# Kernel optimization log

Measured on AMD Instinct MI355X. Metric: run time of the kernel, lower is better.

Reference implementation:

```python
import jax, jax.numpy as jnp
import numpy as np

HEADS = 16
ROPE_BASE = 10000.0


def _rope(x):
    # x: [B, S, D]; rotate interleaved even/odd pairs across full D
    B, S, D = x.shape
    half = D // 2
    inv_freq = 1.0 / (ROPE_BASE ** (jnp.arange(half, dtype=jnp.float32) * 2.0 / D))
    ang = jnp.arange(S, dtype=jnp.float32)[:, None] * inv_freq[None, :]  # [S, half]
    cos, sin = jnp.cos(ang), jnp.sin(ang)
    xp = x.reshape(B, S, half, 2)
    xe, xo = xp[..., 0], xp[..., 1]
    re = xe * cos - xo * sin
    ro = xe * sin + xo * cos
    return jnp.stack([re, ro], axis=-1).reshape(B, S, D)


def setup_inputs() -> dict:
    key = jax.random.key(0)
    ks = jax.random.split(key, 7)
    B, S, D = 2, 2048, 1024
    sc = 1.0 / np.sqrt(D)
    return {
        "queries": jax.random.normal(ks[0], (B, S, D), jnp.float32),
        "keys": jax.random.normal(ks[1], (B, S, D), jnp.float32),
        "values": jax.random.normal(ks[2], (B, S, D), jnp.float32),
        "Wq": jax.random.normal(ks[3], (D, D), jnp.float32) * sc,
        "Wk": jax.random.normal(ks[4], (D, D), jnp.float32) * sc,
        "Wv": jax.random.normal(ks[5], (D, D), jnp.float32) * sc,
        "Wo": jax.random.normal(ks[6], (D, D), jnp.float32) * sc,
    }


def reference(queries, keys, values, Wq, Wk, Wv, Wo):
    B, S, D = queries.shape
    H = HEADS
    dk = D // H
    # bias-free linear projections (torch Linear: x @ W^T)
    q = _rope(queries @ Wq.T)
    k = _rope(keys @ Wk.T)
    v = _rope(values @ Wv.T)
    # split heads: [B, H, S, dk]
    q = q.reshape(B, S, H, dk).transpose(0, 2, 1, 3)
    k = k.reshape(B, S, H, dk).transpose(0, 2, 1, 3)
    v = v.reshape(B, S, H, dk).transpose(0, 2, 1, 3)
    scores = jnp.einsum("bhqd,bhkd->bhqk", q, k) / jnp.sqrt(jnp.float32(dk))
    attn = jax.nn.softmax(scores, axis=-1)
    ctx = jnp.einsum("bhqk,bhkd->bhqd", attn, v)  # [B, H, S, dk]
    z = ctx.transpose(0, 2, 1, 3).reshape(B, S, D)
    return z @ Wo.T
```

## Files before the change

kernel.cpp:

```cpp
#include <hip/hip_runtime.h>
#include <hip/hip_bf16.h>
#include <math.h>


typedef __attribute__((ext_vector_type(8))) short s8v;
typedef __attribute__((ext_vector_type(8))) __bf16 bf16x8;
typedef __attribute__((ext_vector_type(4))) float f32x4;
typedef __attribute__((ext_vector_type(16))) float f32x16;
typedef __attribute__((ext_vector_type(2))) unsigned u32x2;

__device__ inline unsigned short f2bf(float f) {
    unsigned u = __builtin_bit_cast(unsigned, f);
    u += 0x7FFFu + ((u >> 16) & 1u);
    return (unsigned short)(u >> 16);
}

__device__ inline unsigned pk_bf16(float a, float b) {
    __hip_bfloat162 h = __float22bfloat162_rn(float2{a, b});
    unsigned u;
    __builtin_memcpy(&u, &h, 4);
    return u;
}

__device__ inline f32x4 mfma16(s8v a, s8v b, f32x4 c) {
    return __builtin_amdgcn_mfma_f32_16x16x32_bf16(
        __builtin_bit_cast(bf16x8, a), __builtin_bit_cast(bf16x8, b), c, 0, 0, 0);
}

__device__ inline f32x16 mfma32(s8v a, s8v b, f32x16 c) {
    return __builtin_amdgcn_mfma_f32_32x32x16_bf16(
        __builtin_bit_cast(bf16x8, a), __builtin_bit_cast(bf16x8, b), c, 0, 0, 0);
}

struct CvtArgs {
    const float* s[7];
    unsigned short* d[7];
    int n4[7];
};

__global__ __launch_bounds__(256) void cvt_kernel(CvtArgs a) {
    const int which = blockIdx.y;
    const float4* __restrict__ src = (const float4*)a.s[which];
    unsigned short* __restrict__ dst = a.d[which];
    const int n4 = a.n4[which];
    for (int i = blockIdx.x * 256 + threadIdx.x; i < n4; i += gridDim.x * 256) {
        float4 v = src[i];
        uint2 o;
        o.x = pk_bf16(v.x, v.y);
        o.y = pk_bf16(v.z, v.w);
        *(uint2*)(dst + (size_t)i * 4) = o;
    }
}

__global__ __launch_bounds__(256) void rope_table_kernel(float* __restrict__ cosT,
                                                         float* __restrict__ sinT) {
    int i = blockIdx.x * 256 + threadIdx.x;
    int s = i >> 9, d2 = i & 511;
    float inv = exp2f((float)d2 * (-13.287712379549449f / 512.0f));
    float ang = (float)s * inv;
    float sn, cs;
    sincosf(ang, &sn, &cs);
    cosT[i] = cs;
    sinT[i] = sn;
}

struct GemmArgs {
    const unsigned short* A[3];
    const unsigned short* W[3];
    void* C[3];
    const float* cosT;
    const float* sinT;
    float scale[3];
};

template <bool ROPE>
__global__ __launch_bounds__(256) void gemm_bt(GemmArgs g) {
    constexpr int K = 1024, N = 1024;
    const int z = blockIdx.z;
    const unsigned short* __restrict__ A = g.A[z];
    const unsigned short* __restrict__ W = g.W[z];

    const int tid = threadIdx.x;
    const int lane = tid & 63, wid = tid >> 6;
    const int wr = wid >> 1, wc = wid & 1;
    const int row0 = blockIdx.x * 128, col0 = blockIdx.y * 128;
    const int lr = lane & 15, kofs = (lane >> 4) * 8;

    __shared__ __align__(16) unsigned short As[128][72];
    __shared__ __align__(16) unsigned short Ws[128][72];

    f32x4 acc[4][4] = {};

    const int srow = tid >> 3;
    const int schunk = (tid & 7) * 8;

    for (int k0 = 0; k0 < K; k0 += 64) {
        __syncthreads();
#pragma unroll
        for (int i = 0; i < 4; ++i) {
            int r = srow + i * 32;
            *(s8v*)(&As[r][schunk]) =
                *(const s8v*)(A + (size_t)(row0 + r) * K + k0 + schunk);
            *(s8v*)(&Ws[r][schunk]) =
                *(const s8v*)(W + (size_t)(col0 + r) * K + k0 + schunk);
        }
        __syncthreads();

        s8v af[2][4], bf[2][4];
#pragma unroll
        for (int ks = 0; ks < 2; ++ks) {
#pragma unroll
            for (int m = 0; m < 4; ++m)
                af[ks][m] = *(const s8v*)(&As[wr * 64 + m * 16 + lr][ks * 32 + kofs]);
#pragma unroll
            for (int n = 0; n < 4; ++n)
                bf[ks][n] = *(const s8v*)(&Ws[wc * 64 + n * 16 + lr][ks * 32 + kofs]);
        }
#pragma unroll
        for (int m = 0; m < 4; ++m)
#pragma unroll
            for (int n = 0; n < 4; ++n) {
                acc[m][n] = mfma16(af[0][m], bf[0][n], acc[m][n]);
                acc[m][n] = mfma16(af[1][m], bf[1][n], acc[m][n]);
            }
    }

    const int rbase = row0 + wr * 64 + ((lane >> 4) << 2);
    const int cbase = col0 + wc * 64 + lr;
    const float scale = g.scale[z];
#pragma unroll
    for (int m = 0; m < 4; ++m) {
#pragma unroll
        for (int n = 0; n < 4; ++n) {
            const int gc = cbase + n * 16;
#pragma unroll
            for (int r = 0; r < 4; ++r) {
                const int gr = rbase + m * 16 + r;
                float v = acc[m][n][r];
                if constexpr (ROPE) {
                    const int s = gr & 2047;
                    const int d2 = gc >> 1;
                    float cs = g.cosT[s * 512 + d2];
                    float sn = g.sinT[s * 512 + d2];
                    float partner = __shfl_xor(v, 1);
                    v = (v * cs + partner * ((lane & 1) ? sn : -sn)) * scale;
                    ((unsigned short*)g.C[z])[(size_t)gr * N + gc] = f2bf(v);
                } else {
                    ((float*)g.C[z])[(size_t)gr * N + gc] = v;
                }
            }
        }
    }
}

__global__ __launch_bounds__(512, 2) void attn_kernel(
    const unsigned short* __restrict__ Q,
    const unsigned short* __restrict__ Km,
    const unsigned short* __restrict__ Vm,
    unsigned short* __restrict__ ctx) {
    const int tid = threadIdx.x;
    const int lane = tid & 63;
    const int w = tid >> 6;
    const int hi = lane >> 5;
    const int lq = lane & 31;
    const int qt = blockIdx.x;
    const int bh = blockIdx.y;
    const size_t base = (size_t)(bh >> 4) * 2048 * 1024;
    const int hcol = (bh & 15) * 64;
    const int q0 = qt * 256 + w * 32;

    __shared__ __align__(16) unsigned short Vt[2][64][72];

    const int vkey = tid >> 3;
    const int vc = tid & 7;
    const int vphys = ((((vkey >> 3) ^ vc) << 3) | (vkey & 7));

    auto stageV = [&](int buf, s8v vv) {
#pragma unroll
        for (int j = 0; j < 8; ++j)
            Vt[buf][vc * 8 + j][vphys] = (unsigned short)vv[j];
    };

    const unsigned short* __restrict__ Kp = Km + base + (size_t)lq * 1024 + hcol + hi * 8;
    const unsigned short* __restrict__ Vp = Vm + base + (size_t)vkey * 1024 + hcol + vc * 8;

    s8v qf[4];
#pragma unroll
    for (int s = 0; s < 4; ++s)
        qf[s] = *(const s8v*)(Q + base + (size_t)(q0 + lq) * 1024 + hcol + s * 16 + hi * 8);

    s8v kfA[8], kfB[8];
#pragma unroll
    for (int i = 0; i < 8; ++i)
        kfA[i] = *(const s8v*)(Kp + (size_t)((i >> 2) * 32) * 1024 + (i & 3) * 16);

    stageV(0, *(const s8v*)Vp);
    __syncthreads();

    f32x16 accO0 = {}, accO1 = {};
    float lacc = 0.f;

#define ATTN_STEP(KT, CUR, KFC, KFN)                                            \
    {                                                                           \
        const int kt_ = (KT);                                                   \
        const bool pre_ = (kt_ + 64 < 2048);                                    \
        s8v vnxt_;                                                              \
        if (pre_) {                                                             \
            vnxt_ = *(const s8v*)(Vp + (size_t)(kt_ + 64) * 1024);              \
            _Pragma("unroll")                                                   \
            for (int i = 0; i < 8; ++i)                                         \
                KFN[i] = *(const s8v*)(Kp +                                     \
                    (size_t)(kt_ + 64 + (i >> 2) * 32) * 1024 + (i & 3) * 16);  \
        }                                                                       \
                                       \
        f32x16 s0 = {}, s1 = {};                                                \
        _Pragma("unroll")                                                       \
        for (int s = 0; s < 4; ++s) {                                           \
            s0 = mfma32(KFC[s], qf[s], s0);                                     \
            s1 = mfma32(KFC[4 + s], qf[s], s1);                                 \
        }                                                                       \
           \
        s8v vf[8];                                                              \
        _Pragma("unroll")                                                       \
        for (int db = 0; db < 2; ++db)                                          \
            _Pragma("unroll")                                                   \
            for (int ks = 0; ks < 4; ++ks)                                      \
                vf[db * 4 + ks] = *(const s8v*)&Vt[CUR][db * 32 + lq]           \
                    [((2 * ks + hi) ^ ((db * 4 + (lq >> 3)) & 7)) << 3];        \
                                  \
        _Pragma("unroll")                                                       \
        for (int r = 0; r < 16; ++r) {                                          \
            s0[r] = exp2f(s0[r]);                                               \
            s1[r] = exp2f(s1[r]);                                               \
        }                                                                       \
        float t16[16];                                                          \
        _Pragma("unroll")                                                       \
        for (int r = 0; r < 16; ++r) t16[r] = s0[r] + s1[r];                    \
        _Pragma("unroll")                                                       \
        for (int r = 0; r < 8; ++r) t16[r] += t16[r + 8];                       \
        _Pragma("unroll")                                                       \
        for (int r = 0; r < 4; ++r) t16[r] += t16[r + 4];                       \
        lacc += (t16[0] + t16[1]) + (t16[2] + t16[3]);                          \
                                                 \
        unsigned w0[8], w1[8];                                                  \
        _Pragma("unroll")                                                       \
        for (int g = 0; g < 4; ++g) {                                           \
            const int rr = g * 4;                                               \
            w0[g] = pk_bf16(s0[rr], s0[rr + 1]);                                \
            w1[g] = pk_bf16(s0[rr + 2], s0[rr + 3]);                            \
        }                                                                       \
        _Pragma("unroll")                                                       \
        for (int g = 4; g < 8; ++g) {                                           \
            const int rr = (g - 4) * 4;                                         \
            w0[g] = pk_bf16(s1[rr], s1[rr + 1]);                                \
            w1[g] = pk_bf16(s1[rr + 2], s1[rr + 3]);                            \
        }                                                                       \
               \
        s8v pf[4];                                                              \
        _Pragma("unroll")                                                       \
        for (int ks = 0; ks < 4; ++ks) {                                        \
            int4 fi;                                                            \
            PK_SWAP(fi, w0[2 * ks], w0[2 * ks + 1], w1[2 * ks], w1[2 * ks + 1]);\
            pf[ks] = __builtin_bit_cast(s8v, fi);                               \
        }                                                                       \
                                           \
        if (pre_) stageV((CUR) ^ 1, vnxt_);                                     \
        __syncthreads();                                                        \
                                                        \
        _Pragma("unroll")                                                       \
        for (int ks = 0; ks < 4; ++ks) {                                        \
            accO0 = mfma32(vf[ks], pf[ks], accO0);                              \
            accO1 = mfma32(vf[4 + ks], pf[ks], accO1);                          \
        }                                                                       \
    }

#if __has_builtin(__builtin_amdgcn_permlane32_swap)
#define PK_SWAP(fi, a0, b0, a1, b1)                                             \
    {                                                                           \
        u32x2 ra_ = __builtin_amdgcn_permlane32_swap((a0), (b0), false, false); \
        u32x2 rb_ = __builtin_amdgcn_permlane32_swap((a1), (b1), false, false); \
        fi.x = (int)ra_[0]; fi.y = (int)rb_[0];                                 \
        fi.z = (int)ra_[1]; fi.w = (int)rb_[1];                                 \
    }
#else
#define PK_SWAP(fi, a0, b0, a1, b1)                                             \
    {                                                                           \
        unsigned own0 = hi ? (b0) : (a0);                                       \
        unsigned own1 = hi ? (b1) : (a1);                                       \
        unsigned snd0 = hi ? (a0) : (b0);                                       \
        unsigned snd1 = hi ? (a1) : (b1);                                       \
        unsigned rcv0 = (unsigned)__shfl_xor((int)snd0, 32);                    \
        unsigned rcv1 = (unsigned)__shfl_xor((int)snd1, 32);                    \
        fi.x = (int)(hi ? rcv0 : own0);                                         \
        fi.y = (int)(hi ? rcv1 : own1);                                         \
        fi.z = (int)(hi ? own0 : rcv0);                                         \
        fi.w = (int)(hi ? own1 : rcv1);                                         \
    }
#endif

    for (int kt = 0; kt < 2048; kt += 128) {
        ATTN_STEP(kt, 0, kfA, kfB);
        ATTN_STEP(kt + 64, 1, kfB, kfA);
    }
#undef ATTN_STEP
#undef PK_SWAP

    const float ltot = lacc + __shfl_xor(lacc, 32);
    const float rl = 1.0f / ltot;
    unsigned short* dst = ctx + base + (size_t)(q0 + lq) * 1024 + hcol;
#pragma unroll
    for (int r = 0; r < 16; ++r) {
        const int d = (r & 3) + 8 * (r >> 2) + 4 * hi;
        dst[d] = f2bf(accO0[r] * rl);
        dst[d + 32] = f2bf(accO1[r] * rl);
    }
}

extern "C" void kernel_launch(void* const* d_in, const int* in_sizes, int n_in,
                              void* d_out, int out_size, void* d_ws, size_t ws_size,
                              hipStream_t stream) {
    char* ws = (char*)d_ws;
    size_t off = 0;
    auto alloc = [&](size_t bytes) {
        void* p = ws + off;
        off += (bytes + 255) & ~(size_t)255;
        return p;
    };

    const size_t XB = (size_t)4096 * 1024 * 2;
    const size_t WB = (size_t)1024 * 1024 * 2;
    const size_t TB = (size_t)2048 * 512 * 4;

    unsigned short* Xb[3];
    for (int i = 0; i < 3; ++i) Xb[i] = (unsigned short*)alloc(XB);
    unsigned short* Wb[4];
    for (int i = 0; i < 4; ++i) Wb[i] = (unsigned short*)alloc(WB);
    unsigned short* Qb = (unsigned short*)alloc(XB);
    unsigned short* Kb = (unsigned short*)alloc(XB);
    unsigned short* Vb = (unsigned short*)alloc(XB);
    float* cosT = (float*)alloc(TB);
    float* sinT = (float*)alloc(TB);
    unsigned short* ctx = Xb[0];

    CvtArgs ca;
    unsigned short* dsts[7] = {Xb[0], Xb[1], Xb[2], Wb[0], Wb[1], Wb[2], Wb[3]};
    for (int i = 0; i < 7; ++i) {
        ca.s[i] = (const float*)d_in[i];
        ca.d[i] = dsts[i];
        ca.n4[i] = in_sizes[i] / 4;
    }
    cvt_kernel<<<dim3(1024, 7), 256, 0, stream>>>(ca);

    rope_table_kernel<<<4096, 256, 0, stream>>>(cosT, sinT);

    GemmArgs gp;
    gp.A[0] = Xb[0]; gp.A[1] = Xb[1]; gp.A[2] = Xb[2];
    gp.W[0] = Wb[0]; gp.W[1] = Wb[1]; gp.W[2] = Wb[2];
    gp.C[0] = Qb;    gp.C[1] = Kb;    gp.C[2] = Vb;
    gp.cosT = cosT;  gp.sinT = sinT;
    gp.scale[0] = 0.125f * 1.4426950408889634f;
    gp.scale[1] = 1.0f;
    gp.scale[2] = 1.0f;
    gemm_bt<true><<<dim3(32, 8, 3), 256, 0, stream>>>(gp);

    attn_kernel<<<dim3(8, 32), 512, 0, stream>>>(Qb, Kb, Vb, ctx);

    GemmArgs go;
    go.A[0] = ctx;   go.A[1] = ctx;   go.A[2] = ctx;
    go.W[0] = Wb[3]; go.W[1] = Wb[3]; go.W[2] = Wb[3];
    go.C[0] = d_out; go.C[1] = d_out; go.C[2] = d_out;
    go.cosT = cosT;  go.sinT = sinT;
    go.scale[0] = 1.0f; go.scale[1] = 1.0f; go.scale[2] = 1.0f;
    gemm_bt<false><<<dim3(32, 8, 1), 256, 0, stream>>>(go);
}
```

Before: 185.1 us.

## Pre-transpose V in a separate kernel and drop LDS staging in attention

A new kernel writes V transposed per head (d-major, keys contiguous), so the attention kernel can load V fragments straight from global memory. This removes the shared-memory V double buffer and the per-step __syncthreads. The attention blocks shrink from 512 to 256 threads with 128 queries each, the grid is remapped so blocks sharing a head are spread across the flat index, and s_setprio is raised around the MFMA sections. The cost is an extra launch plus a full read and write of V, and every block now fetches V from global or L2 separately.

```diff
diff --git a/kernel.cpp b/kernel.cpp
--- a/kernel.cpp
+++ b/kernel.cpp
@@ -153,36 +153,52 @@
     }
 }
 
-__global__ __launch_bounds__(512, 2) void attn_kernel(
+__global__ __launch_bounds__(256) void transpose_v_kernel(
+    const unsigned short* __restrict__ V, unsigned short* __restrict__ VT) {
+    const int bh = blockIdx.x;
+    const int st = blockIdx.y;
+    const int tid = threadIdx.x;
+    const int b = bh >> 4, h = bh & 15;
+    const int s0 = st * 64;
+    __shared__ __align__(16) unsigned short T[64][72];
+    const int sl = tid >> 3;
+    const int dc = (tid & 7) * 8;
+#pragma unroll
+    for (int i = 0; i < 2; ++i) {
+        const int s = sl + i * 32;
+        s8v v = *(const s8v*)(V + (size_t)(b * 2048 + s0 + s) * 1024 + h * 64 + dc);
+#pragma unroll
+        for (int j = 0; j < 8; ++j) T[dc + j][s] = (unsigned short)v[j];
+    }
+    __syncthreads();
+#pragma unroll
+    for (int i = 0; i < 2; ++i) {
+        const int d = sl + i * 32;
+        s8v r = *(const s8v*)&T[d][dc];
+        *(s8v*)(VT + (size_t)(bh * 64 + d) * 2048 + s0 + dc) = r;
+    }
+}
+
+__global__ __launch_bounds__(256, 2) void attn_kernel(
     const unsigned short* __restrict__ Q,
     const unsigned short* __restrict__ Km,
-    const unsigned short* __restrict__ Vm,
+    const unsigned short* __restrict__ VT,
     unsigned short* __restrict__ ctx) {
     const int tid = threadIdx.x;
     const int lane = tid & 63;
     const int w = tid >> 6;
     const int hi = lane >> 5;
     const int lq = lane & 31;
-    const int qt = blockIdx.x;
-    const int bh = blockIdx.y;
+    const int flat = blockIdx.x;
+    const int vid = (flat & 7) * 64 + (flat >> 3);
+    const int qt = vid & 15;
+    const int bh = vid >> 4;
     const size_t base = (size_t)(bh >> 4) * 2048 * 1024;
     const int hcol = (bh & 15) * 64;
-    const int q0 = qt * 256 + w * 32;
-
-    __shared__ __align__(16) unsigned short Vt[2][64][72];
-
-    const int vkey = tid >> 3;
-    const int vc = tid & 7;
-    const int vphys = ((((vkey >> 3) ^ vc) << 3) | (vkey & 7));
-
-    auto stageV = [&](int buf, s8v vv) {
-#pragma unroll
-        for (int j = 0; j < 8; ++j)
-            Vt[buf][vc * 8 + j][vphys] = (unsigned short)vv[j];
-    };
+    const int q0 = qt * 128 + w * 32;
 
     const unsigned short* __restrict__ Kp = Km + base + (size_t)lq * 1024 + hcol + hi * 8;
-    const unsigned short* __restrict__ Vp = Vm + base + (size_t)vkey * 1024 + hcol + vc * 8;
+    const unsigned short* __restrict__ Vp = VT + (size_t)(bh * 64 + lq) * 2048 + hi * 8;
 
     s8v qf[4];
 #pragma unroll
@@ -194,39 +210,37 @@
     for (int i = 0; i < 8; ++i)
         kfA[i] = *(const s8v*)(Kp + (size_t)((i >> 2) * 32) * 1024 + (i & 3) * 16);
 
-    stageV(0, *(const s8v*)Vp);
-    __syncthreads();
-
     f32x16 accO0 = {}, accO1 = {};
     float lacc = 0.f;
 
-#define ATTN_STEP(KT, CUR, KFC, KFN)                                            \
+#define ATTN_STEP(KT, KFC, KFN)                                                 \
     {                                                                           \
         const int kt_ = (KT);                                                   \
         const bool pre_ = (kt_ + 64 < 2048);                                    \
-        s8v vnxt_;                                                              \
+             \
         if (pre_) {                                                             \
-            vnxt_ = *(const s8v*)(Vp + (size_t)(kt_ + 64) * 1024);              \
             _Pragma("unroll")                                                   \
             for (int i = 0; i < 8; ++i)                                         \
                 KFN[i] = *(const s8v*)(Kp +                                     \
                     (size_t)(kt_ + 64 + (i >> 2) * 32) * 1024 + (i & 3) * 16);  \
         }                                                                       \
+         \
+        s8v vf[8];                                                              \
+        _Pragma("unroll")                                                       \
+        for (int db = 0; db < 2; ++db)                                          \
+            _Pragma("unroll")                                                   \
+            for (int ks = 0; ks < 4; ++ks)                                      \
+                vf[db * 4 + ks] = *(const s8v*)(Vp +                            \
+                    (size_t)(db * 32) * 2048 + kt_ + ks * 16);                  \
                                        \
         f32x16 s0 = {}, s1 = {};                                                \
+        __builtin_amdgcn_s_setprio(1);                                          \
         _Pragma("unroll")                                                       \
         for (int s = 0; s < 4; ++s) {                                           \
             s0 = mfma32(KFC[s], qf[s], s0);                                     \
             s1 = mfma32(KFC[4 + s], qf[s], s1);                                 \
         }                                                                       \
-           \
-        s8v vf[8];                                                              \
-        _Pragma("unroll")                                                       \
-        for (int db = 0; db < 2; ++db)                                          \
-            _Pragma("unroll")                                                   \
-            for (int ks = 0; ks < 4; ++ks)                                      \
-                vf[db * 4 + ks] = *(const s8v*)&Vt[CUR][db * 32 + lq]           \
-                    [((2 * ks + hi) ^ ((db * 4 + (lq >> 3)) & 7)) << 3];        \
+        __builtin_amdgcn_s_setprio(0);                                          \
                                   \
         _Pragma("unroll")                                                       \
         for (int r = 0; r < 16; ++r) {                                          \
@@ -263,15 +277,14 @@
             PK_SWAP(fi, w0[2 * ks], w0[2 * ks + 1], w1[2 * ks], w1[2 * ks + 1]);\
             pf[ks] = __builtin_bit_cast(s8v, fi);                               \
         }                                                                       \
-                                           \
-        if (pre_) stageV((CUR) ^ 1, vnxt_);                                     \
-        __syncthreads();                                                        \
                                                         \
+        __builtin_amdgcn_s_setprio(1);                                          \
         _Pragma("unroll")                                                       \
         for (int ks = 0; ks < 4; ++ks) {                                        \
             accO0 = mfma32(vf[ks], pf[ks], accO0);                              \
             accO1 = mfma32(vf[4 + ks], pf[ks], accO1);                          \
         }                                                                       \
+        __builtin_amdgcn_s_setprio(0);                                          \
     }
 
 #if __has_builtin(__builtin_amdgcn_permlane32_swap)
@@ -299,8 +312,8 @@
 #endif
 
     for (int kt = 0; kt < 2048; kt += 128) {
-        ATTN_STEP(kt, 0, kfA, kfB);
-        ATTN_STEP(kt + 64, 1, kfB, kfA);
+        ATTN_STEP(kt, kfA, kfB);
+        ATTN_STEP(kt + 64, kfB, kfA);
     }
 #undef ATTN_STEP
 #undef PK_SWAP
@@ -338,6 +351,7 @@
     unsigned short* Qb = (unsigned short*)alloc(XB);
     unsigned short* Kb = (unsigned short*)alloc(XB);
     unsigned short* Vb = (unsigned short*)alloc(XB);
+    unsigned short* VTb = (unsigned short*)alloc(XB);
     float* cosT = (float*)alloc(TB);
     float* sinT = (float*)alloc(TB);
     unsigned short* ctx = Xb[0];
@@ -363,7 +377,9 @@
     gp.scale[2] = 1.0f;
     gemm_bt<true><<<dim3(32, 8, 3), 256, 0, stream>>>(gp);
 
-    attn_kernel<<<dim3(8, 32), 512, 0, stream>>>(Qb, Kb, Vb, ctx);
+    transpose_v_kernel<<<dim3(32, 32), 256, 0, stream>>>(Vb, VTb);
+
+    attn_kernel<<<512, 256, 0, stream>>>(Qb, Kb, VTb, ctx);
 
     GemmArgs go;
     go.A[0] = ctx;   go.A[1] = ctx;   go.A[2] = ctx;
```

Result: slower. 214.3 us (+15.8%).
